# Kernel optimization log

Measured on AMD Instinct MI355X. Metric: run time of the kernel, lower is better.

Reference implementation:

```python
import jax, jax.numpy as jnp
import numpy as np
from jax import lax

TD_MAX = 2000
STRIDE = 100


def setup_inputs() -> dict:
    key = jax.random.key(0)
    x = jax.random.normal(key, (20000, 512, 3), dtype=jnp.float32)
    return {"x": x}


def reference(x) -> jnp.ndarray:
    # x: [T, N, 3] trajectory (2D input would be reshaped to [T, -1, 3])
    if x.ndim == 2:
        x = x.reshape(x.shape[0], -1, 3)
    T = x.shape[0]
    N3 = x.shape[1] * x.shape[2]
    t0s = jnp.arange(0, T - TD_MAX, STRIDE)  # time origins, stride 100

    def step(msd, t0):
        # window of td_max frames starting at t0: [td_max, N, 3]
        w = lax.dynamic_slice(x, (t0, 0, 0), (TD_MAX, x.shape[1], x.shape[2]))
        d = w - w[0]                       # displacement from origin frame
        msd = msd + jnp.sum(d * d, axis=(1, 2)) / N3
        return msd, None

    msd0 = jnp.zeros((TD_MAX,), dtype=x.dtype)
    msd, _ = lax.scan(step, msd0, t0s)
    return msd / t0s.shape[0]
```

## Files before the change

kernel.cpp:

```cpp
#include <hip/hip_runtime.h>


typedef __attribute__((ext_vector_type(8))) short bf16x8;
typedef __attribute__((ext_vector_type(4))) float f32x4;

#define ROWF   1536
#define NFRAME 20000
#define NORIG  180
#define WIN    20
#define FB     32
#define NFB    625
#define NKC    2
#define KC     768
#define NKS    24
#define SLOTS  640
#define TDMAX  2000
#define SCALE  (1.0f / (1536.0f * 180.0f))

static __device__ __forceinline__ short f2bf(float f) {
    unsigned u = __builtin_bit_cast(unsigned, f);
    u += 0x7fffu + ((u >> 16) & 1u);
    return (short)(u >> 16);
}

static __device__ __forceinline__ bf16x8 pack8(const float4& v0, const float4& v1) {
    bf16x8 r;
    r[0] = f2bf(v0.x); r[1] = f2bf(v0.y); r[2] = f2bf(v0.z); r[3] = f2bf(v0.w);
    r[4] = f2bf(v1.x); r[5] = f2bf(v1.y); r[6] = f2bf(v1.z); r[7] = f2bf(v1.w);
    return r;
}

static __device__ __forceinline__ float sum8sq(const float4& v0, const float4& v1) {
    return v0.x*v0.x + v0.y*v0.y + v0.z*v0.z + v0.w*v0.w
         + v1.x*v1.x + v1.y*v1.y + v1.z*v1.z + v1.w*v1.w;
}

__global__ __launch_bounds__(256)
void msd_dot_kernel(const float* __restrict__ x, float* __restrict__ ws) {
    __shared__ float sS[FB];
    __shared__ float sO[32];

    const int fb   = blockIdx.x >> 1;
    const int kc   = blockIdx.x & 1;
    const int t0   = fb * FB;
    const int lane = threadIdx.x & 63;
    const int w    = threadIdx.x >> 6;
    const int mt   = w >> 1;
    const int nt   = w & 1;
    const int m    = lane & 15;
    const int quad = lane >> 4;

    const int cmin = t0 / 100;
    int iBase = cmin - (WIN - 1); if (iBase < 0) iBase = 0;

    const int t    = t0 + 16 * mt + m;
    const int iNom = iBase + 16 * nt + m;
    const int iClp = (iNom < NORIG) ? iNom : (NORIG - 1);

    const float* pA = x + (size_t)t * ROWF + kc * KC + quad * 8;
    const float* pB = x + (size_t)(iClp * 100) * ROWF + kc * KC + quad * 8;

    f32x4 acc = {};
    float sAp = 0.0f, sBp = 0.0f;

    #pragma unroll 4
    for (int ks = 0; ks < NKS; ++ks) {
        const float4 a0 = *(const float4*)(pA + ks * 32);
        const float4 a1 = *(const float4*)(pA + ks * 32 + 4);
        const float4 b0 = *(const float4*)(pB + ks * 32);
        const float4 b1 = *(const float4*)(pB + ks * 32 + 4);
        sAp += sum8sq(a0, a1);
        sBp += sum8sq(b0, b1);
        acc = __builtin_amdgcn_mfma_f32_16x16x32_bf16(pack8(a0, a1), pack8(b0, b1),
                                                      acc, 0, 0, 0);
    }

    sAp += __shfl_xor(sAp, 16, 64); sAp += __shfl_xor(sAp, 32, 64);
    sBp += __shfl_xor(sBp, 16, 64); sBp += __shfl_xor(sBp, 32, 64);
    if (lane < 16) { sS[16 * mt + m] = sAp; sO[16 * nt + m] = sBp; }
    __syncthreads();

    float* wsb = ws + (size_t)blockIdx.x * SLOTS;
    #pragma unroll
    for (int r = 0; r < 4; ++r) {
        const int j  = 16 * mt + quad * 4 + r;
        const int tt = t0 + j;
        const int c  = tt / 100;
        const int i  = iBase + 16 * nt + m;
        const int k  = c - i;
        if (k >= 0 && k < WIN && i < NORIG) {
            wsb[k * FB + j] = sS[j] + sO[16 * nt + m] - 2.0f * acc[r];
        }
    }
}

__global__ __launch_bounds__(64)
void msd_reduce_kernel(const float* __restrict__ ws, float* __restrict__ out) {
    const int td   = blockIdx.x;
    const int lane = threadIdx.x;
    const int k    = td / 100;

    float acc = 0.0f;
    #pragma unroll 1
    for (int i = lane; i < NORIG; i += 64) {
        const int t  = 100 * i + td;
        const int fb = t >> 5;
        const int sl = k * FB + (t & 31);
        acc += ws[(size_t)(fb * 2 + 0) * SLOTS + sl];
        acc += ws[(size_t)(fb * 2 + 1) * SLOTS + sl];
    }
    #pragma unroll
    for (int off = 32; off >= 1; off >>= 1)
        acc += __shfl_xor(acc, off, 64);
    if (lane == 0) out[td] = acc * SCALE;
}

extern "C" void kernel_launch(void* const* d_in, const int* in_sizes, int n_in,
                              void* d_out, int out_size, void* d_ws, size_t ws_size,
                              hipStream_t stream) {
    const float* x = (const float*)d_in[0];
    float* out = (float*)d_out;
    float* ws  = (float*)d_ws;

    msd_dot_kernel<<<NFB * NKC, 256, 0, stream>>>(x, ws);
    msd_reduce_kernel<<<TDMAX, 64, 0, stream>>>(ws, out);
}
```

Baseline: 204.9 us.

## Split K dimension into four chunks and fully unroll dot loop

```diff
diff --git a/kernel.cpp b/kernel.cpp
--- a/kernel.cpp
+++ b/kernel.cpp
@@ -10,9 +10,9 @@
 #define WIN    20
 #define FB     32
 #define NFB    625
-#define NKC    2
-#define KC     768
-#define NKS    24
+#define NKC    4
+#define KC     384
+#define NKS    12
 #define SLOTS  640
 #define TDMAX  2000
 #define SCALE  (1.0f / (1536.0f * 180.0f))
@@ -35,13 +35,13 @@
          + v1.x*v1.x + v1.y*v1.y + v1.z*v1.z + v1.w*v1.w;
 }
 
-__global__ __launch_bounds__(256)
+__global__ __launch_bounds__(256, 8)
 void msd_dot_kernel(const float* __restrict__ x, float* __restrict__ ws) {
     __shared__ float sS[FB];
     __shared__ float sO[32];
 
-    const int fb   = blockIdx.x >> 1;
-    const int kc   = blockIdx.x & 1;
+    const int fb   = blockIdx.x >> 2;
+    const int kc   = blockIdx.x & 3;
     const int t0   = fb * FB;
     const int lane = threadIdx.x & 63;
     const int w    = threadIdx.x >> 6;
@@ -63,15 +63,26 @@
     f32x4 acc = {};
     float sAp = 0.0f, sBp = 0.0f;
 
-    #pragma unroll 4
-    for (int ks = 0; ks < NKS; ++ks) {
-        const float4 a0 = *(const float4*)(pA + ks * 32);
-        const float4 a1 = *(const float4*)(pA + ks * 32 + 4);
-        const float4 b0 = *(const float4*)(pB + ks * 32);
-        const float4 b1 = *(const float4*)(pB + ks * 32 + 4);
-        sAp += sum8sq(a0, a1);
-        sBp += sum8sq(b0, b1);
-        acc = __builtin_amdgcn_mfma_f32_16x16x32_bf16(pack8(a0, a1), pack8(b0, b1),
+    #pragma unroll
+    for (int g = 0; g < NKS / 2; ++g) {
+        const float* qA = pA + g * 64;
+        const float* qB = pB + g * 64;
+        const float4 a00 = *(const float4*)(qA);
+        const float4 a01 = *(const float4*)(qA + 4);
+        const float4 b00 = *(const float4*)(qB);
+        const float4 b01 = *(const float4*)(qB + 4);
+        const float4 a10 = *(const float4*)(qA + 32);
+        const float4 a11 = *(const float4*)(qA + 36);
+        const float4 b10 = *(const float4*)(qB + 32);
+        const float4 b11 = *(const float4*)(qB + 36);
+
+        sAp += sum8sq(a00, a01);
+        sBp += sum8sq(b00, b01);
+        acc = __builtin_amdgcn_mfma_f32_16x16x32_bf16(pack8(a00, a01), pack8(b00, b01),
+                                                      acc, 0, 0, 0);
+        sAp += sum8sq(a10, a11);
+        sBp += sum8sq(b10, b11);
+        acc = __builtin_amdgcn_mfma_f32_16x16x32_bf16(pack8(a10, a11), pack8(b10, b11),
                                                       acc, 0, 0, 0);
     }
 
@@ -101,13 +112,19 @@
     const int k    = td / 100;
 
     float acc = 0.0f;
-    #pragma unroll 1
-    for (int i = lane; i < NORIG; i += 64) {
-        const int t  = 100 * i + td;
-        const int fb = t >> 5;
-        const int sl = k * FB + (t & 31);
-        acc += ws[(size_t)(fb * 2 + 0) * SLOTS + sl];
-        acc += ws[(size_t)(fb * 2 + 1) * SLOTS + sl];
+    #pragma unroll
+    for (int ii = 0; ii < 3; ++ii) {
+        const int i = lane + ii * 64;
+        if (i < NORIG) {
+            const int t  = 100 * i + td;
+            const int fb = t >> 5;
+            const int sl = k * FB + (t & 31);
+            const float* base = ws + (size_t)(fb * NKC) * SLOTS + sl;
+            acc += base[0 * SLOTS];
+            acc += base[1 * SLOTS];
+            acc += base[2 * SLOTS];
+            acc += base[3 * SLOTS];
+        }
     }
     #pragma unroll
     for (int off = 32; off >= 1; off >>= 1)
```

After: 477.2 us. +132.9%, slower.
